# Performance work log

Measured on AMD Instinct MI355X. Metric: run time of the kernel, lower is better.

## Reference

```python
import jax, jax.numpy as jnp
import numpy as np
from jax import lax

B, CIN, L, COUT, K = 64, 64, 4096, 128, 7
STRIDE, PAD = 1, 3
POOL, POOL_STRIDE = 2, 2
BN_EPS = 1e-5


def setup_inputs() -> dict:
    key = jax.random.key(0)
    ks = jax.random.split(key, 7)
    I = jax.random.normal(ks[0], (B, CIN, L), jnp.float32)
    bn_gamma = 1.0 + 0.1 * jax.random.normal(ks[1], (CIN,), jnp.float32)
    bn_beta = 0.1 * jax.random.normal(ks[2], (CIN,), jnp.float32)
    bn_mean = 0.1 * jax.random.normal(ks[3], (CIN,), jnp.float32)
    bn_var = jax.random.uniform(ks[4], (CIN,), jnp.float32, 0.5, 1.5)
    conv_w = 0.05 * jax.random.normal(ks[5], (COUT, CIN, K), jnp.float32)
    # XNOR-Net style per-output-channel scale alpha = mean(|W|) over (Cin, K)
    alpha = jnp.mean(jnp.abs(conv_w), axis=(1, 2))  # [COUT]
    prelu_w = jnp.full((1,), 0.25, jnp.float32)  # nn.PReLU() default: 1 shared param
    return dict(I=I, bn_gamma=bn_gamma, bn_beta=bn_beta, bn_mean=bn_mean,
                bn_var=bn_var, conv_w=conv_w, alpha=alpha, prelu_w=prelu_w)


def reference(I, bn_gamma, bn_beta, bn_mean, bn_var, conv_w, alpha, prelu_w):
    # BatchNorm1d (eval mode: running stats), per-channel over dim 1
    scale = (bn_gamma / jnp.sqrt(bn_var + BN_EPS))[None, :, None]
    x = (I - bn_mean[None, :, None]) * scale + bn_beta[None, :, None]
    # Binarize (sign; sign(0)=0 matches torch.sign)
    x = jnp.sign(x)
    # Conv1d, no bias, zero padding=3, stride=1  -> [B, COUT, L]
    y = lax.conv_general_dilated(x, conv_w, window_strides=(STRIDE,),
                                 padding=[(PAD, PAD)],
                                 dimension_numbers=('NCH', 'OIH', 'NCH'))
    # alpha scale (per output channel)
    y = y * alpha[None, :, None]
    # PReLU with single shared parameter
    y = jnp.where(y > 0, y, prelu_w[0] * y)
    # MaxPool1d(kernel=2, stride=2)
    y = lax.reduce_window(y, -jnp.inf, lax.max,
                          (1, 1, POOL), (1, 1, POOL_STRIDE), 'VALID')
    return y
```

## Files before the change

### kernel.cpp

```cpp
#include <hip/hip_runtime.h>
#include <hip/hip_bf16.h>
#include <stdint.h>

#define BATCH 64
#define CIN   64
#define LEN   4096
#define COUT  128
#define KW    7
#define LPOOL 2048

typedef __bf16 v8bf __attribute__((ext_vector_type(8)));
typedef float  v4f  __attribute__((ext_vector_type(4)));

__global__ __launch_bounds__(256)
void wconv_kernel(const float* __restrict__ W, ushort* __restrict__ Wt) {
    int i = blockIdx.x * 256 + threadIdx.x;
    if (i >= COUT * CIN * KW) return;
    int co  = i / (CIN * KW);
    int rem = i - co * (CIN * KW);
    int ci  = rem / KW;
    int k   = rem - ci * KW;
    uint u = __float_as_uint(W[i]);
    uint r = (u + 0x7FFFu + ((u >> 16) & 1u)) >> 16;
    Wt[(k * COUT + co) * CIN + ci] = (ushort)r;
}

__global__ __launch_bounds__(256)
void conv_kernel(const float* __restrict__ I,
                 const float* __restrict__ bn_g, const float* __restrict__ bn_b,
                 const float* __restrict__ bn_m, const float* __restrict__ bn_v,
                 const ushort* __restrict__ Wt,
                 const float* __restrict__ alpha, const float* __restrict__ prelu,
                 float* __restrict__ out) {
    __shared__ __align__(16) char lds_raw[18432];
    ushort* stg = (ushort*)lds_raw;
    float*  ep  = (float*)lds_raw;
    __shared__ float sc_s[CIN], mu_s[CIN], be_s[CIN];

    int tid = threadIdx.x;
    int b = blockIdx.y, l0 = blockIdx.x * 64;

    if (tid < CIN) {
        float s = __fdiv_rn(bn_g[tid], __fsqrt_rn(__fadd_rn(bn_v[tid], 1e-5f)));
        sc_s[tid] = s; mu_s[tid] = bn_m[tid]; be_s[tid] = bn_b[tid];
    }
    __syncthreads();

    const float* Ib = I + (size_t)b * CIN * LEN;
    for (int i = tid; i < CIN * 70; i += 256) {
        int ci = i / 70;
        int r  = i - ci * 70;
        int p  = l0 - 3 + r;
        ushort s = 0;
        if (p >= 0 && p < LEN) {
            float v = Ib[ci * LEN + p];
            float x = __fadd_rn(__fmul_rn(__fsub_rn(v, mu_s[ci]), sc_s[ci]), be_s[ci]);
            s = x > 0.f ? (ushort)0x3F80 : (x < 0.f ? (ushort)0xBF80 : (ushort)0);
        }
        stg[r * 72 + ci] = s;
    }
    __syncthreads();

    int lane = tid & 63, wave = tid >> 6;
    int quad = lane >> 4, lr = lane & 15;
    int cout0 = wave * 32;

    v4f acc[4][2];
    #pragma unroll
    for (int mt = 0; mt < 4; ++mt) { acc[mt][0] = (v4f)0.f; acc[mt][1] = (v4f)0.f; }

    for (int k = 0; k < KW; ++k) {
        #pragma unroll
        for (int h = 0; h < 2; ++h) {
            int cibase = h * 32 + quad * 8;
            const ushort* wrow = Wt + ((size_t)(k * COUT) + cout0 + lr) * CIN + cibase;
            v8bf bf0 = *(const v8bf*)(wrow);
            v8bf bf1 = *(const v8bf*)(wrow + 16 * CIN);
            #pragma unroll
            for (int mt = 0; mt < 4; ++mt) {
                v8bf a = *(const v8bf*)(stg + (mt * 16 + lr + k) * 72 + cibase);
                acc[mt][0] = __builtin_amdgcn_mfma_f32_16x16x32_bf16(a, bf0, acc[mt][0], 0, 0, 0);
                acc[mt][1] = __builtin_amdgcn_mfma_f32_16x16x32_bf16(a, bf1, acc[mt][1], 0, 0, 0);
            }
        }
    }
    __syncthreads();

    float pw = prelu[0];
    #pragma unroll
    for (int nt = 0; nt < 2; ++nt) {
        int co = cout0 + nt * 16 + lr;
        float al = alpha[co];
        #pragma unroll
        for (int mt = 0; mt < 4; ++mt) {
            float v0 = acc[mt][nt][0] * al; v0 = v0 > 0.f ? v0 : pw * v0;
            float v1 = acc[mt][nt][1] * al; v1 = v1 > 0.f ? v1 : pw * v1;
            float v2 = acc[mt][nt][2] * al; v2 = v2 > 0.f ? v2 : pw * v2;
            float v3 = acc[mt][nt][3] * al; v3 = v3 > 0.f ? v3 : pw * v3;
            int lp = mt * 8 + quad * 2;
            ep[co * 36 + lp]     = fmaxf(v0, v1);
            ep[co * 36 + lp + 1] = fmaxf(v2, v3);
        }
    }
    __syncthreads();

    float* ob = out + ((size_t)b * COUT) * LPOOL + blockIdx.x * 32;
    for (int i = tid; i < COUT * 8; i += 256) {
        int co = i >> 3, c4 = i & 7;
        *(float4*)(ob + (size_t)co * LPOOL + c4 * 4) = *(const float4*)(ep + co * 36 + c4 * 4);
    }
}

extern "C" void kernel_launch(void* const* d_in, const int* in_sizes, int n_in,
                              void* d_out, int out_size, void* d_ws, size_t ws_size,
                              hipStream_t stream) {
    const float* I      = (const float*)d_in[0];
    const float* bn_g   = (const float*)d_in[1];
    const float* bn_b   = (const float*)d_in[2];
    const float* bn_m   = (const float*)d_in[3];
    const float* bn_v   = (const float*)d_in[4];
    const float* conv_w = (const float*)d_in[5];
    const float* alpha  = (const float*)d_in[6];
    const float* prelu  = (const float*)d_in[7];
    float* out = (float*)d_out;

    ushort* Wt = (ushort*)d_ws;

    wconv_kernel<<<(COUT * CIN * KW + 255) / 256, 256, 0, stream>>>(conv_w, Wt);
    dim3 grid(LEN / 64, BATCH);
    conv_kernel<<<grid, 256, 0, stream>>>(I, bn_g, bn_b, bn_m, bn_v, Wt, alpha, prelu, out);
}
```

Measured before the change: 206.9 us.

## Vectorize input staging, drop epilogue LDS round trip, write pooled output directly

The input staging loop is restructured so each thread handles 8 channels at one position. It batches global loads into registers, binarizes them, and writes packed 8-wide bf16 vectors to LDS instead of scalar ushorts. The staging window is shifted by one row to align to 72 rows, and the k loop is fully unrolled. The epilogue no longer transposes through LDS with two barriers; each lane stores float2 pooled results straight to global memory, at the cost of narrower, less coalesced stores. Launch bounds now request 4 blocks per CU.

Result: faster. 187.0 us (-9.6%).

```diff
diff --git a/kernel.cpp b/kernel.cpp
--- a/kernel.cpp
+++ b/kernel.cpp
@@ -8,8 +8,10 @@
 #define COUT  128
 #define KW    7
 #define LPOOL 2048
+#define RROWS 72
 
 typedef __bf16 v8bf __attribute__((ext_vector_type(8)));
+typedef unsigned short v8us __attribute__((ext_vector_type(8)));
 typedef float  v4f  __attribute__((ext_vector_type(4)));
 
 __global__ __launch_bounds__(256)
@@ -25,39 +27,60 @@
     Wt[(k * COUT + co) * CIN + ci] = (ushort)r;
 }
 
-__global__ __launch_bounds__(256)
+__global__ __launch_bounds__(256, 4)
 void conv_kernel(const float* __restrict__ I,
                  const float* __restrict__ bn_g, const float* __restrict__ bn_b,
                  const float* __restrict__ bn_m, const float* __restrict__ bn_v,
                  const ushort* __restrict__ Wt,
                  const float* __restrict__ alpha, const float* __restrict__ prelu,
                  float* __restrict__ out) {
-    __shared__ __align__(16) char lds_raw[18432];
-    ushort* stg = (ushort*)lds_raw;
-    float*  ep  = (float*)lds_raw;
-    __shared__ float sc_s[CIN], mu_s[CIN], be_s[CIN];
+    __shared__ __align__(16) ushort stg[RROWS * 72];
+    __shared__ float4 bnc[CIN];
 
     int tid = threadIdx.x;
     int b = blockIdx.y, l0 = blockIdx.x * 64;
 
     if (tid < CIN) {
         float s = __fdiv_rn(bn_g[tid], __fsqrt_rn(__fadd_rn(bn_v[tid], 1e-5f)));
-        sc_s[tid] = s; mu_s[tid] = bn_m[tid]; be_s[tid] = bn_b[tid];
+        bnc[tid] = make_float4(s, bn_m[tid], bn_b[tid], 0.f);
     }
     __syncthreads();
 
-    const float* Ib = I + (size_t)b * CIN * LEN;
-    for (int i = tid; i < CIN * 70; i += 256) {
-        int ci = i / 70;
-        int r  = i - ci * 70;
-        int p  = l0 - 3 + r;
-        ushort s = 0;
-        if (p >= 0 && p < LEN) {
-            float v = Ib[ci * LEN + p];
-            float x = __fadd_rn(__fmul_rn(__fsub_rn(v, mu_s[ci]), sc_s[ci]), be_s[ci]);
-            s = x > 0.f ? (ushort)0x3F80 : (x < 0.f ? (ushort)0xBF80 : (ushort)0);
+    int g = tid >> 5;
+    int rbase = tid & 31;
+    float sc[8], mu[8], be[8];
+    #pragma unroll
+    for (int j = 0; j < 8; ++j) {
+        float4 c = bnc[8 * g + j];
+        sc[j] = c.x; mu[j] = c.y; be[j] = c.z;
+    }
+
+    const float* Ib = I + (size_t)b * CIN * LEN + (size_t)g * 8 * LEN;
+    float v[3][8];
+    bool inb[3];
+    #pragma unroll
+    for (int it = 0; it < 3; ++it) {
+        int r = rbase + 32 * it;
+        int p = l0 - 4 + r;
+        inb[it] = (r < RROWS) && (p >= 0) && (p < LEN);
+        #pragma unroll
+        for (int j = 0; j < 8; ++j)
+            v[it][j] = inb[it] ? Ib[j * LEN + p] : 0.f;
+    }
+    #pragma unroll
+    for (int it = 0; it < 3; ++it) {
+        int r = rbase + 32 * it;
+        if (r < RROWS) {
+            v8us u;
+            #pragma unroll
+            for (int j = 0; j < 8; ++j) {
+                float x = __fadd_rn(__fmul_rn(__fsub_rn(v[it][j], mu[j]), sc[j]), be[j]);
+                ushort s = x > 0.f ? (ushort)0x3F80 : (x < 0.f ? (ushort)0xBF80 : (ushort)0);
+                if (!inb[it]) s = 0;
+                u[j] = s;
+            }
+            *(v8us*)(stg + r * 72 + g * 8) = u;
         }
-        stg[r * 72 + ci] = s;
     }
     __syncthreads();
 
@@ -69,45 +92,38 @@
     #pragma unroll
     for (int mt = 0; mt < 4; ++mt) { acc[mt][0] = (v4f)0.f; acc[mt][1] = (v4f)0.f; }
 
+    #pragma unroll
     for (int k = 0; k < KW; ++k) {
         #pragma unroll
         for (int h = 0; h < 2; ++h) {
             int cibase = h * 32 + quad * 8;
             const ushort* wrow = Wt + ((size_t)(k * COUT) + cout0 + lr) * CIN + cibase;
-            v8bf bf0 = *(const v8bf*)(wrow);
-            v8bf bf1 = *(const v8bf*)(wrow + 16 * CIN);
+            v8bf b0 = *(const v8bf*)(wrow);
+            v8bf b1 = *(const v8bf*)(wrow + 16 * CIN);
             #pragma unroll
             for (int mt = 0; mt < 4; ++mt) {
-                v8bf a = *(const v8bf*)(stg + (mt * 16 + lr + k) * 72 + cibase);
-                acc[mt][0] = __builtin_amdgcn_mfma_f32_16x16x32_bf16(a, bf0, acc[mt][0], 0, 0, 0);
-                acc[mt][1] = __builtin_amdgcn_mfma_f32_16x16x32_bf16(a, bf1, acc[mt][1], 0, 0, 0);
+                v8bf a = *(const v8bf*)(stg + (mt * 16 + lr + k + 1) * 72 + cibase);
+                acc[mt][0] = __builtin_amdgcn_mfma_f32_16x16x32_bf16(a, b0, acc[mt][0], 0, 0, 0);
+                acc[mt][1] = __builtin_amdgcn_mfma_f32_16x16x32_bf16(a, b1, acc[mt][1], 0, 0, 0);
             }
         }
     }
-    __syncthreads();
 
     float pw = prelu[0];
+    float* ob = out + ((size_t)b * COUT) * LPOOL + blockIdx.x * 32;
     #pragma unroll
     for (int nt = 0; nt < 2; ++nt) {
         int co = cout0 + nt * 16 + lr;
         float al = alpha[co];
+        float* oc = ob + (size_t)co * LPOOL + quad * 2;
         #pragma unroll
         for (int mt = 0; mt < 4; ++mt) {
             float v0 = acc[mt][nt][0] * al; v0 = v0 > 0.f ? v0 : pw * v0;
             float v1 = acc[mt][nt][1] * al; v1 = v1 > 0.f ? v1 : pw * v1;
             float v2 = acc[mt][nt][2] * al; v2 = v2 > 0.f ? v2 : pw * v2;
             float v3 = acc[mt][nt][3] * al; v3 = v3 > 0.f ? v3 : pw * v3;
-            int lp = mt * 8 + quad * 2;
-            ep[co * 36 + lp]     = fmaxf(v0, v1);
-            ep[co * 36 + lp + 1] = fmaxf(v2, v3);
+            *(float2*)(oc + mt * 8) = make_float2(fmaxf(v0, v1), fmaxf(v2, v3));
         }
-    }
-    __syncthreads();
-
-    float* ob = out + ((size_t)b * COUT) * LPOOL + blockIdx.x * 32;
-    for (int i = tid; i < COUT * 8; i += 256) {
-        int co = i >> 3, c4 = i & 7;
-        *(float4*)(ob + (size_t)co * LPOOL + c4 * 4) = *(const float4*)(ep + co * 36 + c4 * 4);
     }
 }
 
```
